# Optimization experiments

Hardware: AMD Instinct MI355X
Metric: run time of the kernel (lower is better)

Reference implementation:

```python
import jax, jax.numpy as jnp
import numpy as np

C = 16        # channel_n
HIDDEN = 128  # hidden_size
IN_CH = 3     # input_channels (frozen by forward's concat)
SOBEL_DX = jnp.asarray(np.outer([1, 2, 1], [-1, 0, 1]) / 8.0, jnp.float32)
SOBEL_DY = SOBEL_DX.T


def setup_inputs() -> dict:
    key = jax.random.key(0)
    ks = jax.random.split(key, 9)
    B, H, W, steps = 32, 128, 128, 32
    x = jax.random.normal(ks[0], (B, H, W, C), jnp.float32)
    # precomputed stochastic fire masks: (rand > fire_rate) as float, one per step
    masks = (jax.random.uniform(ks[1], (steps, B, H, W, 1)) > 0.5).astype(jnp.float32)

    def lin(k, fan_in, shape):
        lim = 1.0 / np.sqrt(fan_in)
        return jax.random.uniform(k, shape, jnp.float32, -lim, lim)

    fc0_w = lin(ks[2], 3 * C, (HIDDEN, 3 * C))
    fc0_b = lin(ks[3], 3 * C, (HIDDEN,))
    # torch zero-inits fc1; use small random weights so the update is nontrivial
    fc1_w = lin(ks[4], HIDDEN, (C, HIDDEN)) * 0.1
    fc2_w = lin(ks[5], C, (128, C))
    fc2_b = lin(ks[6], C, (128,))
    fc3_w = lin(ks[7], 128, (13, 128))
    fc3_b = lin(ks[8], 128, (13,))
    return dict(x=x, masks=masks, fc0_w=fc0_w, fc0_b=fc0_b, fc1_w=fc1_w,
                fc2_w=fc2_w, fc2_b=fc2_b, fc3_w=fc3_w, fc3_b=fc3_b, steps=steps)


def _dwconv(x, k):
    # depthwise 3x3 conv, zero ('SAME') padding as in F.conv2d(padding=1)
    kern = jnp.broadcast_to(k[:, :, None, None], (3, 3, 1, C)).astype(x.dtype)
    return jax.lax.conv_general_dilated(
        x, kern, (1, 1), 'SAME',
        dimension_numbers=('NHWC', 'HWIO', 'NHWC'), feature_group_count=C)


def _nca_forward(x, masks, fc0_w, fc0_b, fc1_w, fc2_w, fc2_b, fc3_w, fc3_b):
    # first IN_CH channels are held fixed by the forward loop's concat
    ch_mask = jnp.concatenate(
        [jnp.zeros((IN_CH,), x.dtype), jnp.ones((C - IN_CH,), x.dtype)])

    def step(xc, m):
        y = jnp.concatenate([xc, _dwconv(xc, SOBEL_DX), _dwconv(xc, SOBEL_DY)], axis=-1)  # [B,H,W,3C]
        h = jax.nn.relu(jnp.einsum('bhwc,oc->bhwo', y, fc0_w) + fc0_b)                   # [B,H,W,HIDDEN]
        d = jnp.einsum('bhwo,co->bhwc', h, fc1_w) * m                                    # stochastic update
        return xc + d * ch_mask, None

    xf, _ = jax.lax.scan(step, x, masks)
    pooled = xf.mean(axis=(1, 2))                              # [B,C]
    out = jax.nn.relu(pooled @ fc2_w.T + fc2_b) @ fc3_w.T + fc3_b  # [B,13]
    return out, xf


def reference(x, masks, fc0_w, fc0_b, fc1_w, fc2_w, fc2_b, fc3_w, fc3_b, steps):
    return _nca_forward(x, masks[:steps], fc0_w, fc0_b, fc1_w, fc2_w, fc2_b, fc3_w, fc3_b)
```

## Files before the change

### kernel.cpp

```cpp
#include <hip/hip_runtime.h>

#define CH     16
#define HID    128
#define HWDIM  128
#define NB     32
#define NSTEPS 32

typedef float    f32x4 __attribute__((ext_vector_type(4)));
typedef _Float16 f16x8 __attribute__((ext_vector_type(8)));

#define MEMBAR() asm volatile("" ::: "memory")

__global__ __launch_bounds__(256) void nca_prepack(
    const float* __restrict__ w0, const float* __restrict__ b0,
    const float* __restrict__ w1,
    _Float16* __restrict__ pw0, _Float16* __restrict__ pw1, float* __restrict__ pb0)
{
    const int tid = threadIdx.x;
    for (int s = tid; s < 16 * 64; s += 256) {
        const int f = s >> 6, l = s & 63;
        const int n = f >> 1, ks = f & 1;
        const int o = 16 * n + (l & 15);
        f16x8 v;
        #pragma unroll
        for (int j = 0; j < 8; ++j) {
            const int k = 32 * ks + 8 * (l >> 4) + j;
            v[j] = (_Float16)(k < 48 ? w0[o * 48 + k] : 0.f);
        }
        *reinterpret_cast<f16x8*>(&pw0[s * 8]) = v;
    }
    for (int s = tid; s < 4 * 64; s += 256) {
        const int ks = s >> 6, l = s & 63;
        f16x8 v;
        #pragma unroll
        for (int j = 0; j < 8; ++j) {
            const int k = 32 * ks + 8 * (l >> 4) + j;
            v[j] = (_Float16)w1[(l & 15) * 128 + k];
        }
        *reinterpret_cast<f16x8*>(&pw1[s * 8]) = v;
    }
    for (int s = tid; s < 8 * 64; s += 256)
        pb0[s] = b0[16 * (s >> 6) + (s & 15)];
}

__global__ __launch_bounds__(256, 4) void nca_step(
    const float* __restrict__ xin, float* __restrict__ xout,
    const float* __restrict__ mask,
    const _Float16* __restrict__ pw0, const float* __restrict__ pb0,
    const _Float16* __restrict__ pw1)
{
    __shared__ __align__(16) char pool[36864];
    float (*halo)[18][20] = reinterpret_cast<float(*)[18][20]>(pool);

    const int bz = blockIdx.z;
    const int y0 = blockIdx.y * 16, x0 = blockIdx.x * 16;
    const int tid = threadIdx.x;

    for (int q = tid; q < 18 * 18 * 4; q += 256) {
        const int c4 = q & 3, p = q >> 2;
        const int ii = p / 18, jj = p - ii * 18;
        const int gy = y0 - 1 + ii, gx = x0 - 1 + jj;
        f32x4 v = {0.f, 0.f, 0.f, 0.f};
        if ((unsigned)gy < HWDIM && (unsigned)gx < HWDIM)
            v = *reinterpret_cast<const f32x4*>(
                &xin[(((size_t)bz * HWDIM + gy) * HWDIM + gx) * CH + 4 * c4]);
        *reinterpret_cast<f32x4*>(&halo[ii][jj][4 * c4]) = v;
    }
    __syncthreads();

    const int j = tid & 15, i = tid >> 4;
    const int li = i + 1, lj = j + 1;

    _Float16 idv[16], dxv[16], dyv[16];
    #pragma unroll
    for (int c4 = 0; c4 < 4; ++c4) {
        #define HLD(dy, dx) (*reinterpret_cast<const f32x4*>(&halo[li + (dy)][lj + (dx)][4 * c4]))
        const f32x4 n00 = HLD(-1,-1), n01 = HLD(-1,0), n02 = HLD(-1,1);
        const f32x4 n10 = HLD( 0,-1), n11 = HLD( 0,0), n12 = HLD( 0,1);
        const f32x4 n20 = HLD( 1,-1), n21 = HLD( 1,0), n22 = HLD( 1,1);
        #undef HLD
        const f32x4 gx = ((n02 - n00) + 2.f * (n12 - n10) + (n22 - n20)) * 0.125f;
        const f32x4 gy = ((n20 - n00) + 2.f * (n21 - n01) + (n22 - n02)) * 0.125f;
        #pragma unroll
        for (int e = 0; e < 4; ++e) {
            idv[4 * c4 + e] = (_Float16)n11[e];
            dxv[4 * c4 + e] = (_Float16)gx[e];
            dyv[4 * c4 + e] = (_Float16)gy[e];
        }
    }
    const size_t pix = ((size_t)bz * HWDIM + (y0 + i)) * HWDIM + (x0 + j);
    const float m = mask[pix];
    __syncthreads();

    const int w = tid >> 6, l = tid & 63;
    const int lr = l & 15,  g = l >> 4;
    char* wreg = pool + w * 9216;

    {
        _Float16* yrow = reinterpret_cast<_Float16*>(wreg + l * 144);
        f16x8 v;
        #pragma unroll
        for (int e = 0; e < 8; ++e) v[e] = idv[e];
        *reinterpret_cast<f16x8*>(&yrow[0]) = v;
        #pragma unroll
        for (int e = 0; e < 8; ++e) v[e] = idv[8 + e];
        *reinterpret_cast<f16x8*>(&yrow[8]) = v;
        #pragma unroll
        for (int e = 0; e < 8; ++e) v[e] = dxv[e];
        *reinterpret_cast<f16x8*>(&yrow[16]) = v;
        #pragma unroll
        for (int e = 0; e < 8; ++e) v[e] = dxv[8 + e];
        *reinterpret_cast<f16x8*>(&yrow[24]) = v;
        #pragma unroll
        for (int e = 0; e < 8; ++e) v[e] = dyv[e];
        *reinterpret_cast<f16x8*>(&yrow[32]) = v;
        #pragma unroll
        for (int e = 0; e < 8; ++e) v[e] = dyv[8 + e];
        *reinterpret_cast<f16x8*>(&yrow[40]) = v;
        f16x8 z;
        #pragma unroll
        for (int e = 0; e < 8; ++e) z[e] = (_Float16)0.f;
        *reinterpret_cast<f16x8*>(&yrow[48]) = z;
        *reinterpret_cast<f16x8*>(&yrow[56]) = z;
    }
    MEMBAR();

    f16x8 afrag[8];
    #pragma unroll
    for (int t = 0; t < 4; ++t)
        #pragma unroll
        for (int ks = 0; ks < 2; ++ks)
            afrag[2 * t + ks] = *reinterpret_cast<const f16x8*>(
                wreg + (16 * t + lr) * 144 + 64 * ks + 16 * g);
    MEMBAR();

    f16x8 b1f[4];
    #pragma unroll
    for (int ks = 0; ks < 4; ++ks)
        b1f[ks] = *reinterpret_cast<const f16x8*>(&pw1[(ks * 64 + l) * 8]);
    float bias_n[8];
    #pragma unroll
    for (int n = 0; n < 8; ++n) bias_n[n] = pb0[n * 64 + l];

    f32x4 dacc[4];
    #pragma unroll
    for (int t = 0; t < 4; ++t)
        #pragma unroll
        for (int r = 0; r < 4; ++r) dacc[t][r] = 0.f;

    _Float16* hb = reinterpret_cast<_Float16*>(wreg);
    #pragma unroll
    for (int c = 0; c < 4; ++c) {
        f16x8 b0f[4];
        #pragma unroll
        for (int q = 0; q < 4; ++q)
            b0f[q] = *reinterpret_cast<const f16x8*>(&pw0[((4 * c + q) * 64 + l) * 8]);
        #pragma unroll
        for (int nl = 0; nl < 2; ++nl) {
            const float bo = bias_n[2 * c + nl];
            #pragma unroll
            for (int t = 0; t < 4; ++t) {
                f32x4 acc = {0.f, 0.f, 0.f, 0.f};
                acc = __builtin_amdgcn_mfma_f32_16x16x32_f16(afrag[2*t+0], b0f[2*nl+0], acc, 0, 0, 0);
                acc = __builtin_amdgcn_mfma_f32_16x16x32_f16(afrag[2*t+1], b0f[2*nl+1], acc, 0, 0, 0);
                #pragma unroll
                for (int r = 0; r < 4; ++r)
                    hb[(16 * t + 4 * g + r) * 40 + 16 * nl + lr] =
                        (_Float16)fmaxf(acc[r] + bo, 0.f);
            }
        }
        MEMBAR();
        #pragma unroll
        for (int t = 0; t < 4; ++t)
            dacc[t] = __builtin_amdgcn_mfma_f32_16x16x32_f16(
                *reinterpret_cast<const f16x8*>(&hb[(16 * t + lr) * 40 + 8 * g]),
                b1f[c], dacc[t], 0, 0, 0);
        MEMBAR();
    }

    float* db = reinterpret_cast<float*>(wreg);
    #pragma unroll
    for (int t = 0; t < 4; ++t)
        #pragma unroll
        for (int r = 0; r < 4; ++r)
            db[(16 * t + 4 * g + r) * 20 + lr] = dacc[t][r];
    MEMBAR();

    {
        const float* dp = &db[l * 20];
        const f32x4* xi = reinterpret_cast<const f32x4*>(&xin[pix * CH]);
        f32x4* xo = reinterpret_cast<f32x4*>(&xout[pix * CH]);
        f32x4 dv = *reinterpret_cast<const f32x4*>(&dp[0]);
        f32x4 v0 = xi[0];
        v0[3] += dv[3] * m;
        xo[0] = v0;
        #pragma unroll
        for (int q = 1; q < 4; ++q) {
            f32x4 d4 = *reinterpret_cast<const f32x4*>(&dp[4 * q]);
            f32x4 v  = xi[q];
            #pragma unroll
            for (int e = 0; e < 4; ++e) v[e] += d4[e] * m;
            xo[q] = v;
        }
    }
}

__global__ __launch_bounds__(256) void nca_pool(
    const float* __restrict__ xf, float* __restrict__ partial)
{
    __shared__ float red[256 * CH];
    const int b = blockIdx.x >> 3, part = blockIdx.x & 7, tid = threadIdx.x;
    float acc[CH];
    #pragma unroll
    for (int c = 0; c < CH; ++c) acc[c] = 0.f;
    const int p0 = part * 2048;
    for (int p = p0 + tid; p < p0 + 2048; p += 256) {
        const f32x4* px = reinterpret_cast<const f32x4*>(
            &xf[((size_t)b * HWDIM * HWDIM + p) * CH]);
        #pragma unroll
        for (int q = 0; q < 4; ++q) {
            const f32x4 v = px[q];
            acc[q*4+0] += v[0]; acc[q*4+1] += v[1];
            acc[q*4+2] += v[2]; acc[q*4+3] += v[3];
        }
    }
    #pragma unroll
    for (int c = 0; c < CH; ++c) red[tid * CH + c] = acc[c];
    __syncthreads();
    for (int off = 128; off > 0; off >>= 1) {
        if (tid < off) {
            #pragma unroll
            for (int c = 0; c < CH; ++c)
                red[tid * CH + c] += red[(tid + off) * CH + c];
        }
        __syncthreads();
    }
    if (tid < CH)
        partial[blockIdx.x * CH + tid] = red[tid];
}

__global__ __launch_bounds__(128) void nca_head(
    const float* __restrict__ partial,
    const float* __restrict__ fc2_w, const float* __restrict__ fc2_b,
    const float* __restrict__ fc3_w, const float* __restrict__ fc3_b,
    float* __restrict__ out)
{
    __shared__ float h2[HID];
    __shared__ float pl[CH];
    const int tid = threadIdx.x;
    for (int b = 0; b < NB; ++b) {
        if (tid < CH) {
            float s = 0.f;
            #pragma unroll
            for (int q = 0; q < 8; ++q) s += partial[(b * 8 + q) * CH + tid];
            pl[tid] = s * (1.f / (HWDIM * HWDIM));
        }
        __syncthreads();
        float h = fc2_b[tid];
        #pragma unroll
        for (int c = 0; c < CH; ++c) h += fc2_w[tid * CH + c] * pl[c];
        h2[tid] = fmaxf(h, 0.f);
        __syncthreads();
        if (tid < 13) {
            float o = fc3_b[tid];
            #pragma unroll
            for (int jj = 0; jj < HID; ++jj) o += fc3_w[tid * HID + jj] * h2[jj];
            out[b * 13 + tid] = o;
        }
        __syncthreads();
    }
}

extern "C" void kernel_launch(void* const* d_in, const int* in_sizes, int n_in,
                              void* d_out, int out_size, void* d_ws, size_t ws_size,
                              hipStream_t stream)
{
    const float* x     = (const float*)d_in[0];
    const float* masks = (const float*)d_in[1];
    const float* fc0_w = (const float*)d_in[2];
    const float* fc0_b = (const float*)d_in[3];
    const float* fc1_w = (const float*)d_in[4];
    const float* fc2_w = (const float*)d_in[5];
    const float* fc2_b = (const float*)d_in[6];
    const float* fc3_w = (const float*)d_in[7];
    const float* fc3_b = (const float*)d_in[8];

    float*    out     = (float*)d_out;
    float*    xf      = out + NB * 13;
    float*    buf0    = (float*)d_ws;
    float*    partial = buf0 + (size_t)NB * HWDIM * HWDIM * CH;
    _Float16* pw0     = (_Float16*)(partial + 256 * CH);
    _Float16* pw1     = pw0 + 16 * 64 * 8;
    float*    pb0     = (float*)(pw1 + 4 * 64 * 8);

    nca_prepack<<<1, 256, 0, stream>>>(fc0_w, fc0_b, fc1_w, pw0, pw1, pb0);

    dim3 grid(HWDIM / 16, HWDIM / 16, NB), block(256);
    for (int s = 0; s < NSTEPS; ++s) {
        const float* in = (s == 0) ? x : ((s & 1) ? buf0 : xf);
        float* outp     = (s & 1) ? xf : buf0;
        nca_step<<<grid, block, 0, stream>>>(in, outp,
            masks + (size_t)s * NB * HWDIM * HWDIM, pw0, pb0, pw1);
    }
    nca_pool<<<NB * 8, 256, 0, stream>>>(xf, partial);
    nca_head<<<1, 128, 0, stream>>>(partial, fc2_w, fc2_b, fc3_w, fc3_b, out);
}
```

Baseline: 970.1 us.

## Transpose MFMA operands, vectorize hidden stores, and process two tiles per block

Swaps the A/B operands of both MFMAs so the accumulators come out transposed. This lets the hidden activations be stored as packed f16x4 and the bias be read as f32x4 straight from fc0_b, which removes the prepacked bias buffer. The final update is written directly from the dacc registers, skipping the fp32 LDS staging round-trip. The grid becomes a persistent 1024-block launch where each block loops over two tiles, which adds an extra barrier per tile and halves the number of blocks in flight.

New measurement: 1.444 ms. +48.8%, slower.

```diff
diff --git a/kernel.cpp b/kernel.cpp
--- a/kernel.cpp
+++ b/kernel.cpp
@@ -7,14 +7,14 @@
 #define NSTEPS 32
 
 typedef float    f32x4 __attribute__((ext_vector_type(4)));
+typedef _Float16 f16x4 __attribute__((ext_vector_type(4)));
 typedef _Float16 f16x8 __attribute__((ext_vector_type(8)));
 
 #define MEMBAR() asm volatile("" ::: "memory")
 
 __global__ __launch_bounds__(256) void nca_prepack(
-    const float* __restrict__ w0, const float* __restrict__ b0,
-    const float* __restrict__ w1,
-    _Float16* __restrict__ pw0, _Float16* __restrict__ pw1, float* __restrict__ pb0)
+    const float* __restrict__ w0, const float* __restrict__ w1,
+    _Float16* __restrict__ pw0, _Float16* __restrict__ pw1)
 {
     const int tid = threadIdx.x;
     for (int s = tid; s < 16 * 64; s += 256) {
@@ -39,168 +39,163 @@
         }
         *reinterpret_cast<f16x8*>(&pw1[s * 8]) = v;
     }
-    for (int s = tid; s < 8 * 64; s += 256)
-        pb0[s] = b0[16 * (s >> 6) + (s & 15)];
 }
 
 __global__ __launch_bounds__(256, 4) void nca_step(
     const float* __restrict__ xin, float* __restrict__ xout,
     const float* __restrict__ mask,
-    const _Float16* __restrict__ pw0, const float* __restrict__ pb0,
+    const _Float16* __restrict__ pw0, const float* __restrict__ fc0_b,
     const _Float16* __restrict__ pw1)
 {
     __shared__ __align__(16) char pool[36864];
     float (*halo)[18][20] = reinterpret_cast<float(*)[18][20]>(pool);
 
-    const int bz = blockIdx.z;
-    const int y0 = blockIdx.y * 16, x0 = blockIdx.x * 16;
     const int tid = threadIdx.x;
-
-    for (int q = tid; q < 18 * 18 * 4; q += 256) {
-        const int c4 = q & 3, p = q >> 2;
-        const int ii = p / 18, jj = p - ii * 18;
-        const int gy = y0 - 1 + ii, gx = x0 - 1 + jj;
-        f32x4 v = {0.f, 0.f, 0.f, 0.f};
-        if ((unsigned)gy < HWDIM && (unsigned)gx < HWDIM)
-            v = *reinterpret_cast<const f32x4*>(
-                &xin[(((size_t)bz * HWDIM + gy) * HWDIM + gx) * CH + 4 * c4]);
-        *reinterpret_cast<f32x4*>(&halo[ii][jj][4 * c4]) = v;
-    }
-    __syncthreads();
-
-    const int j = tid & 15, i = tid >> 4;
-    const int li = i + 1, lj = j + 1;
-
-    _Float16 idv[16], dxv[16], dyv[16];
-    #pragma unroll
-    for (int c4 = 0; c4 < 4; ++c4) {
-        #define HLD(dy, dx) (*reinterpret_cast<const f32x4*>(&halo[li + (dy)][lj + (dx)][4 * c4]))
-        const f32x4 n00 = HLD(-1,-1), n01 = HLD(-1,0), n02 = HLD(-1,1);
-        const f32x4 n10 = HLD( 0,-1), n11 = HLD( 0,0), n12 = HLD( 0,1);
-        const f32x4 n20 = HLD( 1,-1), n21 = HLD( 1,0), n22 = HLD( 1,1);
-        #undef HLD
-        const f32x4 gx = ((n02 - n00) + 2.f * (n12 - n10) + (n22 - n20)) * 0.125f;
-        const f32x4 gy = ((n20 - n00) + 2.f * (n21 - n01) + (n22 - n02)) * 0.125f;
-        #pragma unroll
-        for (int e = 0; e < 4; ++e) {
-            idv[4 * c4 + e] = (_Float16)n11[e];
-            dxv[4 * c4 + e] = (_Float16)gx[e];
-            dyv[4 * c4 + e] = (_Float16)gy[e];
-        }
-    }
-    const size_t pix = ((size_t)bz * HWDIM + (y0 + i)) * HWDIM + (x0 + j);
-    const float m = mask[pix];
-    __syncthreads();
-
     const int w = tid >> 6, l = tid & 63;
-    const int lr = l & 15,  g = l >> 4;
-    char* wreg = pool + w * 9216;
-
-    {
-        _Float16* yrow = reinterpret_cast<_Float16*>(wreg + l * 144);
-        f16x8 v;
-        #pragma unroll
-        for (int e = 0; e < 8; ++e) v[e] = idv[e];
-        *reinterpret_cast<f16x8*>(&yrow[0]) = v;
-        #pragma unroll
-        for (int e = 0; e < 8; ++e) v[e] = idv[8 + e];
-        *reinterpret_cast<f16x8*>(&yrow[8]) = v;
-        #pragma unroll
-        for (int e = 0; e < 8; ++e) v[e] = dxv[e];
-        *reinterpret_cast<f16x8*>(&yrow[16]) = v;
-        #pragma unroll
-        for (int e = 0; e < 8; ++e) v[e] = dxv[8 + e];
-        *reinterpret_cast<f16x8*>(&yrow[24]) = v;
-        #pragma unroll
-        for (int e = 0; e < 8; ++e) v[e] = dyv[e];
-        *reinterpret_cast<f16x8*>(&yrow[32]) = v;
-        #pragma unroll
-        for (int e = 0; e < 8; ++e) v[e] = dyv[8 + e];
-        *reinterpret_cast<f16x8*>(&yrow[40]) = v;
-        f16x8 z;
-        #pragma unroll
-        for (int e = 0; e < 8; ++e) z[e] = (_Float16)0.f;
-        *reinterpret_cast<f16x8*>(&yrow[48]) = z;
-        *reinterpret_cast<f16x8*>(&yrow[56]) = z;
-    }
-    MEMBAR();
-
-    f16x8 afrag[8];
-    #pragma unroll
-    for (int t = 0; t < 4; ++t)
-        #pragma unroll
-        for (int ks = 0; ks < 2; ++ks)
-            afrag[2 * t + ks] = *reinterpret_cast<const f16x8*>(
-                wreg + (16 * t + lr) * 144 + 64 * ks + 16 * g);
-    MEMBAR();
-
-    f16x8 b1f[4];
-    #pragma unroll
-    for (int ks = 0; ks < 4; ++ks)
-        b1f[ks] = *reinterpret_cast<const f16x8*>(&pw1[(ks * 64 + l) * 8]);
-    float bias_n[8];
-    #pragma unroll
-    for (int n = 0; n < 8; ++n) bias_n[n] = pb0[n * 64 + l];
-
-    f32x4 dacc[4];
-    #pragma unroll
-    for (int t = 0; t < 4; ++t)
-        #pragma unroll
-        for (int r = 0; r < 4; ++r) dacc[t][r] = 0.f;
-
-    _Float16* hb = reinterpret_cast<_Float16*>(wreg);
-    #pragma unroll
-    for (int c = 0; c < 4; ++c) {
-        f16x8 b0f[4];
-        #pragma unroll
-        for (int q = 0; q < 4; ++q)
-            b0f[q] = *reinterpret_cast<const f16x8*>(&pw0[((4 * c + q) * 64 + l) * 8]);
-        #pragma unroll
-        for (int nl = 0; nl < 2; ++nl) {
-            const float bo = bias_n[2 * c + nl];
-            #pragma unroll
-            for (int t = 0; t < 4; ++t) {
-                f32x4 acc = {0.f, 0.f, 0.f, 0.f};
-                acc = __builtin_amdgcn_mfma_f32_16x16x32_f16(afrag[2*t+0], b0f[2*nl+0], acc, 0, 0, 0);
-                acc = __builtin_amdgcn_mfma_f32_16x16x32_f16(afrag[2*t+1], b0f[2*nl+1], acc, 0, 0, 0);
+    const int lr = l & 15, g = l >> 4;
+
+    #pragma unroll 1
+    for (int rep = 0; rep < 2; ++rep) {
+        const int tile = blockIdx.x + rep * 1024;
+        const int bz = tile >> 6;
+        const int y0 = ((tile >> 3) & 7) * 16, x0 = (tile & 7) * 16;
+
+        __syncthreads();
+
+        for (int q = tid; q < 18 * 18 * 4; q += 256) {
+            const int c4 = q & 3, p = q >> 2;
+            const int ii = p / 18, jj = p - ii * 18;
+            const int gy = y0 - 1 + ii, gx = x0 - 1 + jj;
+            f32x4 v = {0.f, 0.f, 0.f, 0.f};
+            if ((unsigned)gy < HWDIM && (unsigned)gx < HWDIM)
+                v = *reinterpret_cast<const f32x4*>(
+                    &xin[(((size_t)bz * HWDIM + gy) * HWDIM + gx) * CH + 4 * c4]);
+            *reinterpret_cast<f32x4*>(&halo[ii][jj][4 * c4]) = v;
+        }
+        __syncthreads();
+
+        const int j = tid & 15, i = tid >> 4;
+        const int li = i + 1, lj = j + 1;
+        _Float16 idv[16], dxv[16], dyv[16];
+        #pragma unroll
+        for (int c4 = 0; c4 < 4; ++c4) {
+            #define HLD(dy, dx) (*reinterpret_cast<const f32x4*>(&halo[li + (dy)][lj + (dx)][4 * c4]))
+            const f32x4 n00 = HLD(-1,-1), n01 = HLD(-1,0), n02 = HLD(-1,1);
+            const f32x4 n10 = HLD( 0,-1), n11 = HLD( 0,0), n12 = HLD( 0,1);
+            const f32x4 n20 = HLD( 1,-1), n21 = HLD( 1,0), n22 = HLD( 1,1);
+            #undef HLD
+            const f32x4 gx = ((n02 - n00) + 2.f * (n12 - n10) + (n22 - n20)) * 0.125f;
+            const f32x4 gy = ((n20 - n00) + 2.f * (n21 - n01) + (n22 - n02)) * 0.125f;
+            #pragma unroll
+            for (int e = 0; e < 4; ++e) {
+                idv[4 * c4 + e] = (_Float16)n11[e];
+                dxv[4 * c4 + e] = (_Float16)gx[e];
+                dyv[4 * c4 + e] = (_Float16)gy[e];
+            }
+        }
+        __syncthreads();
+
+        char* wreg = pool + w * 9216;
+
+        {
+            _Float16* yrow = reinterpret_cast<_Float16*>(wreg + l * 144);
+            f16x8 v;
+            #pragma unroll
+            for (int e = 0; e < 8; ++e) v[e] = idv[e];
+            *reinterpret_cast<f16x8*>(&yrow[0]) = v;
+            #pragma unroll
+            for (int e = 0; e < 8; ++e) v[e] = idv[8 + e];
+            *reinterpret_cast<f16x8*>(&yrow[8]) = v;
+            #pragma unroll
+            for (int e = 0; e < 8; ++e) v[e] = dxv[e];
+            *reinterpret_cast<f16x8*>(&yrow[16]) = v;
+            #pragma unroll
+            for (int e = 0; e < 8; ++e) v[e] = dxv[8 + e];
+            *reinterpret_cast<f16x8*>(&yrow[24]) = v;
+            #pragma unroll
+            for (int e = 0; e < 8; ++e) v[e] = dyv[e];
+            *reinterpret_cast<f16x8*>(&yrow[32]) = v;
+            #pragma unroll
+            for (int e = 0; e < 8; ++e) v[e] = dyv[8 + e];
+            *reinterpret_cast<f16x8*>(&yrow[40]) = v;
+            f16x8 z;
+            #pragma unroll
+            for (int e = 0; e < 8; ++e) z[e] = (_Float16)0.f;
+            *reinterpret_cast<f16x8*>(&yrow[48]) = z;
+            *reinterpret_cast<f16x8*>(&yrow[56]) = z;
+        }
+        MEMBAR();
+
+        f16x8 afrag[8];
+        #pragma unroll
+        for (int t = 0; t < 4; ++t)
+            #pragma unroll
+            for (int ks = 0; ks < 2; ++ks)
+                afrag[2 * t + ks] = *reinterpret_cast<const f16x8*>(
+                    wreg + (16 * t + lr) * 144 + 64 * ks + 16 * g);
+        MEMBAR();
+
+        f16x8 b1f[4];
+        #pragma unroll
+        for (int ks = 0; ks < 4; ++ks)
+            b1f[ks] = *reinterpret_cast<const f16x8*>(&pw1[(ks * 64 + l) * 8]);
+        f32x4 bq[4][2];
+        #pragma unroll
+        for (int c = 0; c < 4; ++c)
+            #pragma unroll
+            for (int nl = 0; nl < 2; ++nl)
+                bq[c][nl] = *reinterpret_cast<const f32x4*>(&fc0_b[32 * c + 16 * nl + 4 * g]);
+
+        f32x4 dacc[4];
+        #pragma unroll
+        for (int t = 0; t < 4; ++t)
+            #pragma unroll
+            for (int r = 0; r < 4; ++r) dacc[t][r] = 0.f;
+
+        _Float16* hb = reinterpret_cast<_Float16*>(wreg);
+        #pragma unroll
+        for (int c = 0; c < 4; ++c) {
+            f16x8 b0f[4];
+            #pragma unroll
+            for (int q = 0; q < 4; ++q)
+                b0f[q] = *reinterpret_cast<const f16x8*>(&pw0[((4 * c + q) * 64 + l) * 8]);
+            #pragma unroll
+            for (int nl = 0; nl < 2; ++nl) {
                 #pragma unroll
-                for (int r = 0; r < 4; ++r)
-                    hb[(16 * t + 4 * g + r) * 40 + 16 * nl + lr] =
-                        (_Float16)fmaxf(acc[r] + bo, 0.f);
+                for (int t = 0; t < 4; ++t) {
+                    f32x4 acc = {0.f, 0.f, 0.f, 0.f};
+                    acc = __builtin_amdgcn_mfma_f32_16x16x32_f16(b0f[2*nl+0], afrag[2*t+0], acc, 0, 0, 0);
+                    acc = __builtin_amdgcn_mfma_f32_16x16x32_f16(b0f[2*nl+1], afrag[2*t+1], acc, 0, 0, 0);
+                    f16x4 hv;
+                    #pragma unroll
+                    for (int r = 0; r < 4; ++r)
+                        hv[r] = (_Float16)fmaxf(acc[r] + bq[c][nl][r], 0.f);
+                    *reinterpret_cast<f16x4*>(
+                        reinterpret_cast<char*>(hb) + (16 * t + lr) * 80 + 32 * nl + 8 * g) = hv;
+                }
             }
-        }
-        MEMBAR();
-        #pragma unroll
-        for (int t = 0; t < 4; ++t)
-            dacc[t] = __builtin_amdgcn_mfma_f32_16x16x32_f16(
-                *reinterpret_cast<const f16x8*>(&hb[(16 * t + lr) * 40 + 8 * g]),
-                b1f[c], dacc[t], 0, 0, 0);
-        MEMBAR();
-    }
-
-    float* db = reinterpret_cast<float*>(wreg);
-    #pragma unroll
-    for (int t = 0; t < 4; ++t)
-        #pragma unroll
-        for (int r = 0; r < 4; ++r)
-            db[(16 * t + 4 * g + r) * 20 + lr] = dacc[t][r];
-    MEMBAR();
-
-    {
-        const float* dp = &db[l * 20];
-        const f32x4* xi = reinterpret_cast<const f32x4*>(&xin[pix * CH]);
-        f32x4* xo = reinterpret_cast<f32x4*>(&xout[pix * CH]);
-        f32x4 dv = *reinterpret_cast<const f32x4*>(&dp[0]);
-        f32x4 v0 = xi[0];
-        v0[3] += dv[3] * m;
-        xo[0] = v0;
-        #pragma unroll
-        for (int q = 1; q < 4; ++q) {
-            f32x4 d4 = *reinterpret_cast<const f32x4*>(&dp[4 * q]);
-            f32x4 v  = xi[q];
-            #pragma unroll
-            for (int e = 0; e < 4; ++e) v[e] += d4[e] * m;
-            xo[q] = v;
+            MEMBAR();
+            #pragma unroll
+            for (int t = 0; t < 4; ++t)
+                dacc[t] = __builtin_amdgcn_mfma_f32_16x16x32_f16(
+                    b1f[c],
+                    *reinterpret_cast<const f16x8*>(
+                        reinterpret_cast<const char*>(hb) + (16 * t + lr) * 80 + 16 * g),
+                    dacc[t], 0, 0, 0);
+            MEMBAR();
+        }
+
+        #pragma unroll
+        for (int t = 0; t < 4; ++t) {
+            const size_t pix = ((size_t)bz * HWDIM + (y0 + 4 * w + t)) * HWDIM + (x0 + lr);
+            const float m = mask[pix];
+            const f32x4 xi = *reinterpret_cast<const f32x4*>(&xin[pix * CH + 4 * g]);
+            f32x4 d4 = dacc[t];
+            if (g == 0) { d4[0] = 0.f; d4[1] = 0.f; d4[2] = 0.f; }
+            f32x4 o;
+            #pragma unroll
+            for (int e = 0; e < 4; ++e) o[e] = xi[e] + d4[e] * m;
+            *reinterpret_cast<f32x4*>(&xout[pix * CH + 4 * g]) = o;
         }
     }
 }
@@ -291,16 +286,14 @@
     float*    partial = buf0 + (size_t)NB * HWDIM * HWDIM * CH;
     _Float16* pw0     = (_Float16*)(partial + 256 * CH);
     _Float16* pw1     = pw0 + 16 * 64 * 8;
-    float*    pb0     = (float*)(pw1 + 4 * 64 * 8);
-
-    nca_prepack<<<1, 256, 0, stream>>>(fc0_w, fc0_b, fc1_w, pw0, pw1, pb0);
-
-    dim3 grid(HWDIM / 16, HWDIM / 16, NB), block(256);
+
+    nca_prepack<<<1, 256, 0, stream>>>(fc0_w, fc1_w, pw0, pw1);
+
     for (int s = 0; s < NSTEPS; ++s) {
         const float* in = (s == 0) ? x : ((s & 1) ? buf0 : xf);
         float* outp     = (s & 1) ? xf : buf0;
-        nca_step<<<grid, block, 0, stream>>>(in, outp,
-            masks + (size_t)s * NB * HWDIM * HWDIM, pw0, pb0, pw1);
+        nca_step<<<1024, 256, 0, stream>>>(in, outp,
+            masks + (size_t)s * NB * HWDIM * HWDIM, pw0, fc0_b, pw1);
     }
     nca_pool<<<NB * 8, 256, 0, stream>>>(xf, partial);
     nca_head<<<1, 128, 0, stream>>>(partial, fc2_w, fc2_b, fc3_w, fc3_b, out);
```
